# Kernel tuning notes

Measured on AMD Instinct MI355X. Metric: run time of the kernel, lower is better.

## Reference

```python
import jax, jax.numpy as jnp
import numpy as np

BETA = 0.25  # commitment-loss weight (kwargs['beta'])


def setup_inputs() -> dict:
    key = jax.random.key(0)
    k1, k2 = jax.random.split(key)
    B, C, H, W = 16, 256, 64, 64
    K = 2048
    feats = jax.random.normal(k1, (B, C, H, W), dtype=jnp.float32)
    # nn.Embedding init: uniform(-1/n_codewords, 1/codeword_dim)
    codebook = jax.random.uniform(k2, (K, C), minval=-1.0 / K, maxval=1.0 / C,
                                  dtype=jnp.float32)
    return {"feats": feats, "codebook": codebook}


def reference(feats, codebook):
    B, C, H, W = feats.shape
    K = codebook.shape[0]
    z = jnp.transpose(feats, (0, 2, 3, 1))          # [B,H,W,C]
    zf = z.reshape(-1, C)                            # [N,C], N=B*H*W
    # squared-euclidean distances via ||z||^2 + ||e||^2 - 2 z.e : [N,K]
    d = (jnp.sum(zf * zf, axis=1, keepdims=True)
         + jnp.sum(codebook * codebook, axis=1)
         - 2.0 * (zf @ codebook.T))
    min_encoding_indices = jnp.argmin(d, axis=1)     # [N]
    mat_id_probs = jax.nn.softmax(-jnp.abs(d), axis=1)  # [N,K]
    z_q = codebook[min_encoding_indices].reshape(z.shape)  # [B,H,W,C]
    loss = (BETA * jnp.mean((jax.lax.stop_gradient(z_q) - z) ** 2)
            + jnp.mean((z_q - jax.lax.stop_gradient(z)) ** 2))
    # straight-through estimator
    z_q_st = z + jax.lax.stop_gradient(z_q - z)
    z_q_out = jnp.transpose(z_q_st, (0, 3, 1, 2))    # [B,C,H,W]
    idx_out = min_encoding_indices.reshape(B, H, W)
    probs_out = jnp.transpose(mat_id_probs.reshape(B, H, W, K), (0, 3, 1, 2))
    return z_q_out, idx_out, loss, probs_out
```

## Files before the change

### kernel.cpp

```cpp
#include <hip/hip_runtime.h>

#define HW 4096
#define CC 256
#define KK 2048
#define BB 16
#define NN (BB*HW)
#define RPB 128

#define ZQ_SZ   (BB*CC*HW)
#define IDX_OFF ZQ_SZ
#define LOSS_OFF (IDX_OFF + NN)
#define PROBS_OFF (LOSS_OFF + 1)

#define EH_OFF 0
#define EE_OFF 262144

#define TAU 0.01f
#define CAND_CAP 512
#define KTC 64
#define KT_N 32

typedef short bf16x8 __attribute__((ext_vector_type(8)));
typedef float f32x16 __attribute__((ext_vector_type(16)));
typedef unsigned int u32;
typedef unsigned long long u64;

__device__ __forceinline__ void gload16(const void* g, void* l){
  __builtin_amdgcn_global_load_lds(
      (const __attribute__((address_space(1))) u32*)g,
      (__attribute__((address_space(3))) u32*)l, 16, 0, 0);
}

__device__ __forceinline__ unsigned short bf16rn(float x){
  unsigned u = __float_as_uint(x);
  return (unsigned short)((u + 0x7fffu + ((u >> 16) & 1u)) >> 16);
}

template<int STRIDE>
__device__ __forceinline__ float np_sumsq256(const float* __restrict__ a){
  float res0 = 0.f, res1 = 0.f;
  #pragma unroll
  for (int h = 0; h < 2; h++){
    const float* p = a + (size_t)h * 128 * STRIDE;
    float r[8];
    #pragma unroll
    for (int j = 0; j < 8; j++){ float x = p[(size_t)j * STRIDE]; r[j] = __fmul_rn(x, x); }
    for (int i = 8; i < 128; i += 8){
      #pragma unroll
      for (int j = 0; j < 8; j++){
        float x = p[(size_t)(i + j) * STRIDE];
        r[j] = __fadd_rn(r[j], __fmul_rn(x, x));
      }
    }
    float s = __fadd_rn(__fadd_rn(__fadd_rn(r[0], r[1]), __fadd_rn(r[2], r[3])),
                        __fadd_rn(__fadd_rn(r[4], r[5]), __fadd_rn(r[6], r[7])));
    if (h == 0) res0 = s; else res1 = s;
  }
  return __fadd_rn(res0, res1);
}

__global__ void k_cvt(const float* __restrict__ cb, float* __restrict__ out){
  const int i = blockIdx.x * 256 + threadIdx.x;
  const int k = i >> 5, c8 = (i & 31) * 8;
  const float* row = cb + (size_t)k * CC + c8;
  unsigned short v[8];
  #pragma unroll
  for (int j = 0; j < 8; ++j) v[j] = bf16rn(row[j]);
  *(uint4*)((unsigned short*)(out + EH_OFF) + (size_t)k * CC + c8) = *(uint4*)v;
}

__global__ void k_ee(const float* __restrict__ cb, float* __restrict__ out){
  const int k = blockIdx.x * 256 + threadIdx.x;
  out[EE_OFF + k] = np_sumsq256<1>(cb + (size_t)k * CC);
}

__global__ __launch_bounds__(256, 2)
void k_mfma(const float* __restrict__ feats, const float* __restrict__ cb,
            float* __restrict__ out){
  __shared__ __align__(16) unsigned char lds_e[2][32768];
  __shared__ float ee_lds[KK];
  __shared__ unsigned long long rowkey[RPB];
  __shared__ int cand[CAND_CAP];
  __shared__ int cand_n;
  __shared__ float lsum;

  const int t = threadIdx.x;
  const int w = t >> 6, l = t & 63;
  const int grp = l >> 5;
  const int lane31 = l & 31;
  const int n0 = blockIdx.x * RPB;
  const int bi = n0 >> 12;
  const int hw0 = n0 & 4095;
  const int myhw = hw0 + w * 32 + lane31;

  for (int i = t; i < KK; i += 256) ee_lds[i] = out[EE_OFF + i];
  if (t < RPB) rowkey[t] = ~0ull;
  if (t == 0){ cand_n = 0; lsum = 0.f; }

  bf16x8 ah0[16];
  {
    const float* zb = feats + (size_t)bi * CC * HW + myhw;
    #pragma unroll
    for (int cs = 0; cs < 16; ++cs){
      #pragma unroll
      for (int j = 0; j < 8; ++j)
        ah0[cs][j] = (short)bf16rn(zb[(size_t)(cs * 16 + grp * 8 + j) * HW]);
    }
  }

  const unsigned short* ehg = (const unsigned short*)(out + EH_OFF);

  int ofs_[8];
  #pragma unroll
  for (int i = 0; i < 8; ++i){
    int ix = i * 256 + t;
    int cd = ix & 63, g = (ix >> 6) & 1, cs = ix >> 7;
    ofs_[i] = cd * CC + cs * 16 + g * 8;
  }

#define STAGE(KT, B) { \
    const unsigned short* tb_ = ehg + (size_t)(KT) * (KTC * CC); \
    _Pragma("unroll") \
    for (int i_ = 0; i_ < 8; ++i_) \
      gload16(tb_ + ofs_[i_], &lds_e[B][(i_ * 256 + t) * 16]); }

#define COMPUTE(B, AA, AB) { \
    _Pragma("unroll") \
    for (int ii = 0; ii < 16; ++ii){ AA[ii] = 0.f; AB[ii] = 0.f; } \
    _Pragma("unroll") \
    for (int cs = 0; cs < 16; ++cs){ \
      const unsigned char* bp_ = &lds_e[B][(size_t)(cs * 2 + grp) * 1024 + lane31 * 16]; \
      bf16x8 e0_ = *(const bf16x8*)(bp_); \
      bf16x8 e1_ = *(const bf16x8*)(bp_ + 512); \
      AA = __builtin_amdgcn_mfma_f32_32x32x16_bf16(e0_, ah0[cs], AA, 0, 0, 0); \
      AB = __builtin_amdgcn_mfma_f32_32x32x16_bf16(e1_, ah0[cs], AB, 0, 0, 0); \
    } }

#define POST(PKT, PA, PB_) { \
    const int ptt = (PKT) & 31; \
    const int eebase = ptt * 64 + 4 * grp; \
    if ((PKT) < KT_N){ \
      _Pragma("unroll") \
      for (int r = 0; r < 16; ++r){ \
        int off = (r & 3) + 8 * (r >> 2); \
        float s0 = ee_lds[eebase + off]      - 2.f * PA[r]; \
        float s1 = ee_lds[eebase + off + 32] - 2.f * PB_[r]; \
        m0 = fminf(m0, fminf(s0, s1)); \
        ss0 += __expf(-s0) + __expf(-s1); \
      } \
    } else { \
      float* pb = out + (size_t)PROBS_OFF \
                + (size_t)(bi * KK + ptt * 64 + 4 * grp) * HW + myhw; \
      _Pragma("unroll") \
      for (int r = 0; r < 16; ++r){ \
        int off = (r & 3) + 8 * (r >> 2); \
        float s0 = ee_lds[eebase + off]      - 2.f * PA[r]; \
        float s1 = ee_lds[eebase + off + 32] - 2.f * PB_[r]; \
        float* p = pb + (size_t)off * HW; \
        p[0]               = __expf(-s0) * inv0; \
        p[(size_t)32 * HW] = __expf(-s1) * inv0; \
        int cg = eebase + off; \
        if (s0 <= m0 + TAU){ \
          int sl = atomicAdd(&cand_n, 1); \
          if (sl < CAND_CAP) cand[sl] = ((w * 32 + lane31) << 16) | cg; \
        } \
        if (s1 <= m0 + TAU){ \
          int sl = atomicAdd(&cand_n, 1); \
          if (sl < CAND_CAP) cand[sl] = ((w * 32 + lane31) << 16) | (cg + 32); \
        } \
      } \
    } }

  f32x16 aA0, aB0, aA1, aB1;
  float m0 = 3e38f, ss0 = 0.f, inv0 = 0.f;

  STAGE(0, 0);
  __syncthreads();

  for (int kt2 = 0; kt2 < KT_N; ++kt2){
    const int ktA = 2 * kt2;
    {
      STAGE((ktA + 1) & 31, 1);
      if (ktA > 0) POST(ktA - 1, aA1, aB1);
      if (ktA == KT_N){
        m0 = fminf(m0, __shfl_xor(m0, 32));
        ss0 += __shfl_xor(ss0, 32);
        inv0 = 1.f / ss0;
      }
      COMPUTE(0, aA0, aB0);
      __syncthreads();
    }
    {
      const int ktB = ktA + 1;
      if (ktB < 2 * KT_N - 1) STAGE((ktB + 1) & 31, 0);
      POST(ktB - 1, aA0, aB0);
      COMPUTE(1, aA1, aB1);
      __syncthreads();
    }
  }
  POST(2 * KT_N - 1, aA1, aB1);
  __syncthreads();

  int nc = cand_n; if (nc > CAND_CAP) nc = CAND_CAP;
  for (int i = t; i < nc; i += 256){
    int rc = cand[i];
    int rl = (rc >> 16) & 127, code = rc & 2047;
    int n = n0 + rl;
    const float* zp = feats + (size_t)(n >> 12) * CC * HW + (n & 4095);
    const float* ep = cb + (size_t)code * CC;
    float a = 0.f;
    #pragma unroll 8
    for (int c = 0; c < CC; ++c) a = __builtin_fmaf(zp[(size_t)c * HW], ep[c], a);
    float zzv = np_sumsq256<HW>(zp);
    float t1 = __fadd_rn(zzv, ee_lds[code]);
    float d = __fadd_rn(t1, -2.f * a);
    unsigned long long key = ((unsigned long long)__float_as_uint(d) << 32) | (unsigned)code;
    atomicMin(&rowkey[rl], key);
  }
  __syncthreads();

  if (t < RPB) out[IDX_OFF + n0 + t] = (float)(int)(rowkey[t] & 2047u);

  if (t < RPB){
    int code = (int)(rowkey[t] & 2047u);
    const float* ep = cb + (size_t)code * CC;
    const float* zp = feats + (size_t)bi * CC * HW + hw0 + t;
    float s = 0.f;
    for (int c = 0; c < CC; ++c){
      float dz = ep[c] - zp[(size_t)c * HW];
      s = __builtin_fmaf(dz, dz, s);
    }
    atomicAdd(&lsum, s);
  }
  __syncthreads();
  if (t == 0) atomicAdd(out + LOSS_OFF, lsum * (1.25f / 16777216.f));
}

__global__ void k_zq(const float* __restrict__ cb, float* __restrict__ out){
  const int f4 = blockIdx.x * 256 + threadIdx.x;
  const int f = f4 * 4;
  const int b = f >> 20;
  const int rem = f & 1048575;
  const int c = rem >> 12;
  const int hw = rem & 4095;
  const int n = b * HW + hw;
  const float* idxf = out + IDX_OFF;
  float4 iv = *(const float4*)(idxf + n);
  float4 o;
  o.x = cb[(size_t)((int)iv.x) * CC + c];
  o.y = cb[(size_t)((int)iv.y) * CC + c];
  o.z = cb[(size_t)((int)iv.z) * CC + c];
  o.w = cb[(size_t)((int)iv.w) * CC + c];
  *(float4*)(out + f) = o;
}

extern "C" void kernel_launch(void* const* d_in, const int* in_sizes, int n_in,
                              void* d_out, int out_size, void* d_ws, size_t ws_size,
                              hipStream_t stream){
  const float* feats = (const float*)d_in[0];
  const float* cb    = (const float*)d_in[1];
  float* out = (float*)d_out;

  (void)hipMemsetAsync(out + LOSS_OFF, 0, sizeof(float), stream);
  hipLaunchKernelGGL(k_cvt,  dim3(256),   dim3(256), 0, stream, cb, out);
  hipLaunchKernelGGL(k_ee,   dim3(8),     dim3(256), 0, stream, cb, out);
  hipLaunchKernelGGL(k_mfma, dim3(512),   dim3(256), 0, stream, feats, cb, out);
  hipLaunchKernelGGL(k_zq,   dim3(16384), dim3(256), 0, stream, cb, out);
}
```

Before: 460.6 us.

## Use triple-buffered 32-code tiles with vmcnt-gated barriers in MFMA kernel

Halves the codebook tile to 32 codes and moves from double to triple buffering in LDS, staging two tiles ahead. The full __syncthreads after each tile is replaced with s_waitcnt vmcnt plus s_barrier, so the oldest async global-to-LDS loads are awaited while later ones stay in flight. MFMA issue is raised with s_setprio, and the two accumulators now split the K dimension and are summed in the epilogue. The aim is to hide load latency better and reduce stalls at barriers. The cost is twice as many tile iterations and barriers, and correctness rests on hand-tuned vmcnt counts.

```diff
diff --git a/kernel.cpp b/kernel.cpp
--- a/kernel.cpp
+++ b/kernel.cpp
@@ -17,8 +17,9 @@
 
 #define TAU 0.01f
 #define CAND_CAP 512
-#define KTC 64
-#define KT_N 32
+#define KTC 32
+#define KT_N 64
+#define TB 16384
 
 typedef short bf16x8 __attribute__((ext_vector_type(8)));
 typedef float f32x16 __attribute__((ext_vector_type(16)));
@@ -35,6 +36,8 @@
   unsigned u = __float_as_uint(x);
   return (unsigned short)((u + 0x7fffu + ((u >> 16) & 1u)) >> 16);
 }
+
+#define PBW(N) asm volatile("s_waitcnt vmcnt(" N ")\n\ts_barrier" ::: "memory");
 
 template<int STRIDE>
 __device__ __forceinline__ float np_sumsq256(const float* __restrict__ a){
@@ -77,7 +80,7 @@
 __global__ __launch_bounds__(256, 2)
 void k_mfma(const float* __restrict__ feats, const float* __restrict__ cb,
             float* __restrict__ out){
-  __shared__ __align__(16) unsigned char lds_e[2][32768];
+  __shared__ __align__(16) unsigned char lds_e[3 * TB];
   __shared__ float ee_lds[KK];
   __shared__ unsigned long long rowkey[RPB];
   __shared__ int cand[CAND_CAP];
@@ -110,92 +113,92 @@
 
   const unsigned short* ehg = (const unsigned short*)(out + EH_OFF);
 
-  int ofs_[8];
+  int ofs_[4];
   #pragma unroll
-  for (int i = 0; i < 8; ++i){
+  for (int i = 0; i < 4; ++i){
     int ix = i * 256 + t;
-    int cd = ix & 63, g = (ix >> 6) & 1, cs = ix >> 7;
+    int cd = ix & 31, g = (ix >> 5) & 1, cs = ix >> 6;
     ofs_[i] = cd * CC + cs * 16 + g * 8;
   }
 
-#define STAGE(KT, B) { \
+#define STAGE(KT, BI) { \
+    unsigned char* bb_ = lds_e + (size_t)(BI) * TB; \
     const unsigned short* tb_ = ehg + (size_t)(KT) * (KTC * CC); \
     _Pragma("unroll") \
-    for (int i_ = 0; i_ < 8; ++i_) \
-      gload16(tb_ + ofs_[i_], &lds_e[B][(i_ * 256 + t) * 16]); }
-
-#define COMPUTE(B, AA, AB) { \
+    for (int i_ = 0; i_ < 4; ++i_) \
+      gload16(tb_ + ofs_[i_], bb_ + (i_ * 256 + t) * 16); }
+
+#define COMPUTE(BI, AA, AB) { \
+    const unsigned char* hb_ = lds_e + (size_t)(BI) * TB; \
     _Pragma("unroll") \
     for (int ii = 0; ii < 16; ++ii){ AA[ii] = 0.f; AB[ii] = 0.f; } \
+    __builtin_amdgcn_s_setprio(1); \
     _Pragma("unroll") \
     for (int cs = 0; cs < 16; ++cs){ \
-      const unsigned char* bp_ = &lds_e[B][(size_t)(cs * 2 + grp) * 1024 + lane31 * 16]; \
-      bf16x8 e0_ = *(const bf16x8*)(bp_); \
-      bf16x8 e1_ = *(const bf16x8*)(bp_ + 512); \
-      AA = __builtin_amdgcn_mfma_f32_32x32x16_bf16(e0_, ah0[cs], AA, 0, 0, 0); \
-      AB = __builtin_amdgcn_mfma_f32_32x32x16_bf16(e1_, ah0[cs], AB, 0, 0, 0); \
-    } }
+      const unsigned char* bp_ = hb_ + (size_t)(cs * 2 + grp) * 512 + lane31 * 16; \
+      bf16x8 e_ = *(const bf16x8*)(bp_); \
+      if (cs & 1) AB = __builtin_amdgcn_mfma_f32_32x32x16_bf16(e_, ah0[cs], AB, 0, 0, 0); \
+      else        AA = __builtin_amdgcn_mfma_f32_32x32x16_bf16(e_, ah0[cs], AA, 0, 0, 0); \
+    } \
+    __builtin_amdgcn_s_setprio(0); }
 
 #define POST(PKT, PA, PB_) { \
-    const int ptt = (PKT) & 31; \
-    const int eebase = ptt * 64 + 4 * grp; \
+    const int ptt = (PKT) & 63; \
+    const int eebase = ptt * KTC + 4 * grp; \
     if ((PKT) < KT_N){ \
       _Pragma("unroll") \
       for (int r = 0; r < 16; ++r){ \
         int off = (r & 3) + 8 * (r >> 2); \
-        float s0 = ee_lds[eebase + off]      - 2.f * PA[r]; \
-        float s1 = ee_lds[eebase + off + 32] - 2.f * PB_[r]; \
-        m0 = fminf(m0, fminf(s0, s1)); \
-        ss0 += __expf(-s0) + __expf(-s1); \
+        float s = ee_lds[eebase + off] - 2.f * (PA[r] + PB_[r]); \
+        m0 = fminf(m0, s); \
+        ss0 += __expf(-s); \
       } \
     } else { \
       float* pb = out + (size_t)PROBS_OFF \
-                + (size_t)(bi * KK + ptt * 64 + 4 * grp) * HW + myhw; \
+                + (size_t)(bi * KK + eebase) * HW + myhw; \
       _Pragma("unroll") \
       for (int r = 0; r < 16; ++r){ \
         int off = (r & 3) + 8 * (r >> 2); \
-        float s0 = ee_lds[eebase + off]      - 2.f * PA[r]; \
-        float s1 = ee_lds[eebase + off + 32] - 2.f * PB_[r]; \
-        float* p = pb + (size_t)off * HW; \
-        p[0]               = __expf(-s0) * inv0; \
-        p[(size_t)32 * HW] = __expf(-s1) * inv0; \
-        int cg = eebase + off; \
-        if (s0 <= m0 + TAU){ \
+        float s = ee_lds[eebase + off] - 2.f * (PA[r] + PB_[r]); \
+        pb[(size_t)off * HW] = __expf(-s) * inv0; \
+        if (s <= m0 + TAU){ \
           int sl = atomicAdd(&cand_n, 1); \
-          if (sl < CAND_CAP) cand[sl] = ((w * 32 + lane31) << 16) | cg; \
-        } \
-        if (s1 <= m0 + TAU){ \
-          int sl = atomicAdd(&cand_n, 1); \
-          if (sl < CAND_CAP) cand[sl] = ((w * 32 + lane31) << 16) | (cg + 32); \
+          if (sl < CAND_CAP) cand[sl] = ((w * 32 + lane31) << 16) | (eebase + off); \
         } \
       } \
     } }
 
+#define PBSEL(KT) { \
+    if ((KT) >= 125)      { PBW("0") } \
+    else if ((KT) <= 64)  { PBW("4") } \
+    else                  { PBW("20") } }
+
   f32x16 aA0, aB0, aA1, aB1;
   float m0 = 3e38f, ss0 = 0.f, inv0 = 0.f;
 
   STAGE(0, 0);
-  __syncthreads();
+  STAGE(1, 1);
+  PBW("4")
 
   for (int kt2 = 0; kt2 < KT_N; ++kt2){
     const int ktA = 2 * kt2;
     {
-      STAGE((ktA + 1) & 31, 1);
+      if (ktA <= 125) STAGE((ktA + 2) & 63, (ktA + 2) % 3);
       if (ktA > 0) POST(ktA - 1, aA1, aB1);
       if (ktA == KT_N){
         m0 = fminf(m0, __shfl_xor(m0, 32));
         ss0 += __shfl_xor(ss0, 32);
         inv0 = 1.f / ss0;
       }
-      COMPUTE(0, aA0, aB0);
-      __syncthreads();
+      COMPUTE(ktA % 3, aA0, aB0);
+      PBSEL(ktA)
     }
     {
       const int ktB = ktA + 1;
-      if (ktB < 2 * KT_N - 1) STAGE((ktB + 1) & 31, 0);
+      if (ktB <= 125) STAGE((ktB + 2) & 63, (ktB + 2) % 3);
       POST(ktB - 1, aA0, aB0);
-      COMPUTE(1, aA1, aB1);
-      __syncthreads();
+      COMPUTE(ktB % 3, aA1, aB1);
+      PBSEL(ktB)
     }
   }
   POST(2 * KT_N - 1, aA1, aB1);
```

After: 482.0 us. +4.7%, slower.
